# Kernel optimization log

Hardware: AMD Instinct MI355X
Metric: run time of the kernel (lower is better)

Reference implementation:

```python
import jax, jax.numpy as jnp
import numpy as np

NUM_CHANNEL_TYPES = 32  # global channel vocabulary (matches fill_max of channel_idx)


def setup_inputs() -> dict:
    key = jax.random.key(0)
    k1, k2, k3, k4, k5, k6 = jax.random.split(key, 6)
    B, C, H, W, E, P = 32, 8, 224, 224, 768, 16
    return {
        "x": jax.random.normal(k1, (B, C, H, W), dtype=jnp.float32),
        "channel_idx": jax.random.randint(k2, (B, C), 0, NUM_CHANNEL_TYPES, dtype=jnp.int64),
        "proj_w": jax.random.normal(k3, (E, P, P), dtype=jnp.float32) * 0.02,
        "proj_b": jax.random.normal(k4, (E,), dtype=jnp.float32) * 0.02,
        "ctx_w": jax.random.normal(k5, (E, E), dtype=jnp.float32) * 0.02,
        "ctx_b": jax.random.normal(k6, (E,), dtype=jnp.float32) * 0.02,
    }


def reference(x, channel_idx, proj_w, proj_b, ctx_w, ctx_b):
    B, C, H, W = x.shape
    E, P, _ = proj_w.shape
    Hp, Wp = H // P, W // P

    # Conv3d(1, E, kernel=(1,P,P), stride=(1,P,P)) == per-channel 2D patchify matmul
    xp = x.reshape(B, C, Hp, P, Wp, P)
    emb = jnp.einsum('bchpwq,epq->bechw', xp, proj_w) + proj_b[None, :, None, None, None]
    # emb: (B, E, C, Hp, Wp)

    # per-(sample, channel) average patch embedding -> (B, C, E)
    av_patch = emb.mean(axis=(3, 4)).transpose(0, 2, 1)
    flat = av_patch.reshape(B * C, E)
    seg = channel_idx.reshape(-1)

    # segment-mean over the batch by channel index (fused scatter-mean)
    sums = jax.ops.segment_sum(flat, seg, num_segments=NUM_CHANNEL_TYPES)
    cnt = jax.ops.segment_sum(jnp.ones((B * C,), flat.dtype), seg, num_segments=NUM_CHANNEL_TYPES)
    means = sums / jnp.maximum(cnt, 1.0)[:, None]
    chan_embed = means[seg].reshape(B, C, E)  # torch computes this under no_grad

    # context projection and broadcast-add back onto patch embeddings
    ctx = chan_embed @ ctx_w.T + ctx_b            # (B, C, E)
    out = emb + ctx.transpose(0, 2, 1)[:, :, :, None, None]

    # flatten(2).transpose(1, 2): (B, C*Hp*Wp, E)
    return out.reshape(B, E, C * Hp * Wp).transpose(0, 2, 1)
```

## Files before the change

kernel.cpp:

```cpp
#include <hip/hip_runtime.h>
#include <hip/hip_bf16.h>

typedef __attribute__((ext_vector_type(8))) short s16x8;
typedef __attribute__((ext_vector_type(4))) float f32x4;
typedef __attribute__((ext_vector_type(8))) unsigned short u16x8;
typedef __attribute__((ext_vector_type(4))) unsigned short u16x4;

static __device__ __forceinline__ unsigned short f2bf(float f) {
  unsigned int u = __float_as_uint(f);
  unsigned int r = u + 0x7fffu + ((u >> 16) & 1u);
  return (unsigned short)(r >> 16);
}
static __device__ __forceinline__ float bf2f(unsigned short s) {
  return __uint_as_float(((unsigned int)s) << 16);
}

static __device__ __forceinline__ void gload16(const void* g, void* l) {
  __builtin_amdgcn_global_load_lds(
      (const __attribute__((address_space(1))) unsigned int*)g,
      (__attribute__((address_space(3))) unsigned int*)l, 16, 0, 0);
}

__global__ __launch_bounds__(256) void k_mega(const float* __restrict__ x,
                                              unsigned short* __restrict__ xbf,
                                              float* __restrict__ avg3,
                                              const float* __restrict__ pw,
                                              unsigned short* __restrict__ pwbf,
                                              const float* __restrict__ cw,
                                              float* __restrict__ cwT) {
  __shared__ __align__(16) char smem[7168];
  int b = blockIdx.x, t = threadIdx.x;
  if (b < 3584) {
    unsigned short* strip = (unsigned short*)smem;
    int bc = b / 14, hp = b - bc * 14;
    const float* img = x + ((size_t)bc * 224 + hp * 16) * 224;
    for (int idx = t; idx < 896; idx += 256) {
      int row = idx / 56, c4 = idx - row * 56;
      float4 v = reinterpret_cast<const float4*>(img + (size_t)row * 224)[c4];
      int wp = c4 >> 2, q0 = (c4 & 3) << 2;
      u16x4 pk = { f2bf(v.x), f2bf(v.y), f2bf(v.z), f2bf(v.w) };
      *(u16x4*)&strip[wp * 256 + row * 16 + q0] = pk;
    }
    __syncthreads();
    float acc = 0.f;
#pragma unroll
    for (int wp = 0; wp < 14; ++wp) acc += bf2f(strip[wp * 256 + t]);
    avg3[((size_t)bc * 14 + hp) * 256 + t] = acc;
    const u16x8* so = (const u16x8*)strip;
    u16x8* go = (u16x8*)(xbf + ((size_t)bc * 196 + hp * 14) * 256);
    for (int i = t; i < 448; i += 256) go[i] = so[i];
  } else if (b < 3776) {
    int i = (b - 3584) * 256 + t;
    float4 v = reinterpret_cast<const float4*>(pw)[i];
    u16x4 pk = { f2bf(v.x), f2bf(v.y), f2bf(v.z), f2bf(v.w) };
    reinterpret_cast<u16x4*>(pwbf)[i] = pk;
  } else {
    float (*tile)[33] = (float(*)[33])smem;
    int bid2 = b - 3776;
    int bx = bid2 % 24, by = bid2 / 24;
    int tx = t & 31, ty = t >> 5;
#pragma unroll
    for (int k = 0; k < 4; ++k)
      tile[ty + 8 * k][tx] = cw[(size_t)(by * 32 + ty + 8 * k) * 768 + bx * 32 + tx];
    __syncthreads();
#pragma unroll
    for (int k = 0; k < 4; ++k)
      cwT[(size_t)(bx * 32 + ty + 8 * k) * 768 + by * 32 + tx] = tile[tx][ty + 8 * k];
  }
}

__global__ __launch_bounds__(256) void k_segmean(const float* __restrict__ avg3,
                                                 const int* __restrict__ seg,
                                                 float* __restrict__ sp) {
  __shared__ float red[4][64];
  __shared__ int rcnt[4];
  __shared__ int ssg[256];
  int s = blockIdx.x & 31, kc = blockIdx.x >> 5;
  int t = threadIdx.x;
  int kl = t & 63, slice = t >> 6;
  int k = kc * 64 + kl;
  ssg[t] = seg[t];
  __syncthreads();
  float sum = 0.f; int cnt = 0;
  for (int bc = slice * 64; bc < slice * 64 + 64; ++bc) {
    if (ssg[bc] == s) {
      ++cnt;
      const float* row = avg3 + (size_t)bc * 14 * 256 + k;
#pragma unroll
      for (int hp = 0; hp < 14; ++hp) sum += row[hp * 256];
    }
  }
  red[slice][kl] = sum;
  if (kl == 0) rcnt[slice] = cnt;
  __syncthreads();
  if (t < 64) {
    float tot = red[0][t] + red[1][t] + red[2][t] + red[3][t];
    int c = rcnt[0] + rcnt[1] + rcnt[2] + rcnt[3];
    sp[s * 256 + kc * 64 + t] = tot / (196.0f * (float)(c > 0 ? c : 1));
  }
}

__global__ __launch_bounds__(256) void k_means2(const float* __restrict__ sp,
                                                const float* __restrict__ pw,
                                                const float* __restrict__ pb,
                                                float* __restrict__ means) {
  __shared__ float ssp[256];
  __shared__ float red[8][32];
  int s = blockIdx.x & 31, e0 = (blockIdx.x >> 5) << 5;
  int t = threadIdx.x;
  int e = t & 31, ksl = t >> 5;
  ssp[t] = sp[s * 256 + t];
  __syncthreads();
  const float4* w = reinterpret_cast<const float4*>(pw + (size_t)(e0 + e) * 256 + ksl * 32);
  float a = 0.f;
#pragma unroll
  for (int j = 0; j < 8; ++j) {
    float4 v = w[j];
    int kb = ksl * 32 + j * 4;
    a += v.x * ssp[kb] + v.y * ssp[kb + 1] + v.z * ssp[kb + 2] + v.w * ssp[kb + 3];
  }
  red[ksl][e] = a;
  __syncthreads();
  if (t < 32) {
    float tot = 0.f;
#pragma unroll
    for (int j = 0; j < 8; ++j) tot += red[j][t];
    means[s * 768 + e0 + t] = tot + pb[e0 + t];
  }
}

__global__ __launch_bounds__(256) void k_ctx2(const float* __restrict__ means,
                                              const float* __restrict__ cwT,
                                              const float* __restrict__ cb,
                                              const float* __restrict__ pb,
                                              float* __restrict__ addv) {
  __shared__ float mn[768];
  __shared__ float red[8][32];
  int s = blockIdx.x & 31, e0 = (blockIdx.x >> 5) << 5;
  int t = threadIdx.x;
  int e = t & 31, fsl = t >> 5;
  mn[t] = means[s * 768 + t];
  mn[t + 256] = means[s * 768 + 256 + t];
  mn[t + 512] = means[s * 768 + 512 + t];
  __syncthreads();
  const float* col = cwT + (size_t)fsl * 96 * 768 + e0 + e;
  float a = 0.f;
#pragma unroll 8
  for (int j = 0; j < 96; ++j) a += mn[fsl * 96 + j] * col[(size_t)j * 768];
  red[fsl][e] = a;
  __syncthreads();
  if (t < 32) {
    float tot = 0.f;
#pragma unroll
    for (int j = 0; j < 8; ++j) tot += red[j][t];
    addv[s * 768 + e0 + t] = tot + cb[e0 + t] + pb[e0 + t];
  }
}

__global__ __launch_bounds__(256) void k_gemm(
    const unsigned short* __restrict__ xbf, const unsigned short* __restrict__ wbf,
    const float* __restrict__ addv, const int* __restrict__ seg,
    float* __restrict__ out) {
  __shared__ __align__(16) unsigned short Al[128 * 64];
  __shared__ __align__(16) unsigned short Bl[128 * 64];

  int bid = blockIdx.x;
  int xcd = bid & 7, local = bid >> 3;
  int mb = xcd * 49 + local / 6;
  int nb = local - (local / 6) * 6;
  int m0 = mb << 7, n0 = nb << 7;

  int t = threadIdx.x;
  int wave = t >> 6, lane = t & 63;
  int wm = (wave >> 1) << 6, wn = (wave & 1) << 6;
  int lr = lane & 15, hi = lane >> 4;
  int axor = (lr & 7) << 4;

  int swz = (((lane & 7) ^ ((lane >> 3) & 7)) << 4);
  const char* abase = (const char*)xbf + (size_t)(m0 + (lane >> 3)) * 512 + swz + (size_t)wave * 16384;
  const char* bbase = (const char*)wbf + (size_t)(n0 + (lane >> 3)) * 512 + swz + (size_t)wave * 16384;
  char* adst = (char*)Al + wave * 4096;
  char* bdst = (char*)Bl + wave * 4096;
  const char* Alc = (const char*)Al;
  const char* Blc = (const char*)Bl;

  f32x4 acc[4][4] = {};

  for (int kt = 0; kt < 4; ++kt) {
#pragma unroll
    for (int i = 0; i < 4; ++i) {
      gload16(abase + kt * 128 + i * 4096, adst + i * 1024);
      gload16(bbase + kt * 128 + i * 4096, bdst + i * 1024);
    }
    __syncthreads();
#pragma unroll
    for (int kk = 0; kk < 2; ++kk) {
      s16x8 af[4], bv[4];
      int koff = kk * 64 + hi * 16;
#pragma unroll
      for (int i = 0; i < 4; ++i)
        af[i] = *(const s16x8*)(Alc + (wm + i * 16 + lr) * 128 + (koff ^ axor));
#pragma unroll
      for (int j = 0; j < 4; ++j)
        bv[j] = *(const s16x8*)(Blc + (wn + j * 16 + lr) * 128 + (koff ^ axor));
#pragma unroll
      for (int i = 0; i < 4; ++i)
#pragma unroll
        for (int j = 0; j < 4; ++j)
          acc[i][j] = __builtin_amdgcn_mfma_f32_16x16x32_bf16(bv[j], af[i], acc[i][j], 0, 0, 0);
    }
    __syncthreads();
  }

#pragma unroll
  for (int i = 0; i < 4; ++i) {
    int M = m0 + wm + i * 16 + lr;
    int sgi = seg[M / 196];
    const float* av = addv + (size_t)sgi * 768 + n0 + wn + hi * 4;
    float* orow = out + (size_t)M * 768 + n0 + wn + hi * 4;
#pragma unroll
    for (int j = 0; j < 4; ++j) {
      f32x4 a4 = *(const f32x4*)(av + j * 16);
      f32x4 v = acc[i][j];
      v.x += a4.x; v.y += a4.y; v.z += a4.z; v.w += a4.w;
      *(f32x4*)(orow + j * 16) = v;
    }
  }
}

__global__ void k_cvt_fb(const float* __restrict__ in, unsigned short* __restrict__ o) {
  int i = blockIdx.x * 256 + threadIdx.x;
  float4 v = reinterpret_cast<const float4*>(in)[i];
  u16x4 pk = { f2bf(v.x), f2bf(v.y), f2bf(v.z), f2bf(v.w) };
  reinterpret_cast<u16x4*>(o)[i] = pk;
}

__global__ void k_transpose_fb(const float* __restrict__ in, float* __restrict__ out) {
  __shared__ float tile[32][33];
  int bx = blockIdx.x % 24, by = blockIdx.x / 24;
  int tx = threadIdx.x & 31, ty = threadIdx.x >> 5;
#pragma unroll
  for (int k = 0; k < 4; ++k)
    tile[ty + 8 * k][tx] = in[(size_t)(by * 32 + ty + 8 * k) * 768 + bx * 32 + tx];
  __syncthreads();
#pragma unroll
  for (int k = 0; k < 4; ++k)
    out[(size_t)(bx * 32 + ty + 8 * k) * 768 + by * 32 + tx] = tile[tx][ty + 8 * k];
}

__global__ void k_avgpatch_fb(const float* __restrict__ x, float* __restrict__ avg) {
  int bc = blockIdx.x;
  int k = threadIdx.x;
  int p = k >> 4, q = k & 15;
  const float* base = x + (size_t)bc * 224 * 224;
  float s = 0.f;
  for (int hp = 0; hp < 14; ++hp) {
    const float* row = base + (hp * 16 + p) * 224 + q;
#pragma unroll
    for (int wp = 0; wp < 14; ++wp) s += row[wp * 16];
  }
  avg[bc * 256 + k] = s * (1.0f / 196.0f);
}

__global__ __launch_bounds__(768) void k_chain_fb(const float* __restrict__ avg,
                                                  const int* __restrict__ seg,
                                                  const float* __restrict__ pw,
                                                  const float* __restrict__ pb,
                                                  const float* __restrict__ cwT,
                                                  const float* __restrict__ cb,
                                                  float* __restrict__ addv) {
  __shared__ float sp[256];
  __shared__ float mn[768];
  __shared__ int ssg[256];
  int s = blockIdx.x, t = threadIdx.x;
  if (t < 256) ssg[t] = seg[t];
  __syncthreads();
  if (t < 256) {
    float sum = 0.f; int c = 0;
    for (int bc = 0; bc < 256; ++bc)
      if (ssg[bc] == s) { sum += avg[bc * 256 + t]; ++c; }
    sp[t] = sum / (float)(c > 0 ? c : 1);
  }
  __syncthreads();
  {
    const float4* w = reinterpret_cast<const float4*>(pw + (size_t)t * 256);
    float a = 0.f;
#pragma unroll 8
    for (int k = 0; k < 64; ++k) {
      float4 v = w[k];
      a += v.x * sp[k * 4] + v.y * sp[k * 4 + 1] + v.z * sp[k * 4 + 2] + v.w * sp[k * 4 + 3];
    }
    mn[t] = a + pb[t];
  }
  __syncthreads();
  float a2 = 0.f;
#pragma unroll 8
  for (int f = 0; f < 768; ++f) a2 += mn[f] * cwT[(size_t)f * 768 + t];
  addv[s * 768 + t] = a2 + cb[t] + pb[t];
}

__global__ __launch_bounds__(256) void k_gemm_fb(
    const float* __restrict__ x, const unsigned short* __restrict__ wbf,
    const float* __restrict__ addv, const int* __restrict__ seg,
    float* __restrict__ out) {
  __shared__ unsigned short Al[128][40];
  __shared__ unsigned short Bl[128][40];
  int bid = blockIdx.x;
  int xcd = bid & 7, local = bid >> 3;
  int mb = xcd * 49 + local / 6;
  int nb = local - (local / 6) * 6;
  int m0 = mb << 7, n0 = nb << 7;
  int t = threadIdx.x;
  int wave = t >> 6, lane = t & 63;
  int wm = (wave >> 1) << 6, wn = (wave & 1) << 6;
  int lr = lane & 15, lk = (lane >> 4) << 3;
  int mstage = m0 + (t >> 1);
  int halfA = t & 1;
  int bc = mstage / 196;
  int pij = mstage - bc * 196;
  int hp = pij / 14;
  int wp = pij - hp * 14;
  const float* xbase = x + ((size_t)bc * 224 + hp * 16 + halfA) * 224 + wp * 16;
  const unsigned short* bsrc = wbf + (size_t)(n0 + (t >> 1)) * 256 + halfA * 16;
  unsigned short* adst = &Al[t >> 1][halfA * 16];
  unsigned short* bdst = &Bl[t >> 1][halfA * 16];
  f32x4 acc[4][4] = {};
  for (int ks = 0; ks < 8; ++ks) {
    __syncthreads();
    *(u16x8*)bdst       = *(const u16x8*)(bsrc + ks * 32);
    *(u16x8*)(bdst + 8) = *(const u16x8*)(bsrc + ks * 32 + 8);
    {
      const float4* src = reinterpret_cast<const float4*>(xbase + ks * 448);
      float4 v0 = src[0], v1 = src[1], v2 = src[2], v3 = src[3];
      u16x8 p0 = { f2bf(v0.x), f2bf(v0.y), f2bf(v0.z), f2bf(v0.w),
                   f2bf(v1.x), f2bf(v1.y), f2bf(v1.z), f2bf(v1.w) };
      u16x8 p1 = { f2bf(v2.x), f2bf(v2.y), f2bf(v2.z), f2bf(v2.w),
                   f2bf(v3.x), f2bf(v3.y), f2bf(v3.z), f2bf(v3.w) };
      *(u16x8*)adst = p0;
      *(u16x8*)(adst + 8) = p1;
    }
    __syncthreads();
    s16x8 af[4], bfv[4];
#pragma unroll
    for (int i = 0; i < 4; ++i) af[i] = *(const s16x8*)&Al[wm + i * 16 + lr][lk];
#pragma unroll
    for (int j = 0; j < 4; ++j) bfv[j] = *(const s16x8*)&Bl[wn + j * 16 + lr][lk];
#pragma unroll
    for (int i = 0; i < 4; ++i)
#pragma unroll
      for (int j = 0; j < 4; ++j)
        acc[i][j] = __builtin_amdgcn_mfma_f32_16x16x32_bf16(bfv[j], af[i], acc[i][j], 0, 0, 0);
  }
#pragma unroll
  for (int i = 0; i < 4; ++i) {
    int M = m0 + wm + i * 16 + lr;
    int sgi = seg[M / 196];
    int hi = lane >> 4;
    const float* av = addv + (size_t)sgi * 768 + n0 + wn + hi * 4;
    float* orow = out + (size_t)M * 768 + n0 + wn + hi * 4;
#pragma unroll
    for (int j = 0; j < 4; ++j) {
      f32x4 a4 = *(const f32x4*)(av + j * 16);
      f32x4 v = acc[i][j];
      v.x += a4.x; v.y += a4.y; v.z += a4.z; v.w += a4.w;
      *(f32x4*)(orow + j * 16) = v;
    }
  }
}


extern "C" void kernel_launch(void* const* d_in, const int* in_sizes, int n_in,
                              void* d_out, int out_size, void* d_ws, size_t ws_size,
                              hipStream_t stream) {
  (void)in_sizes; (void)n_in; (void)out_size;
  const float* x  = (const float*)d_in[0];
  const int*   sg = (const int*)d_in[1];
  const float* pw = (const float*)d_in[2];
  const float* pb = (const float*)d_in[3];
  const float* cw = (const float*)d_in[4];
  const float* cb = (const float*)d_in[5];
  float* out = (float*)d_out;

  char* ws = (char*)d_ws;
  unsigned short* pwbf = (unsigned short*)ws;
  float* cwT   = (float*)(ws + 393216);
  float* addv  = (float*)(ws + 2752512);
  float* sp    = (float*)(ws + 2850816);
  float* means = (float*)(ws + 2883584);
  float* avg3  = (float*)(ws + 2981888);
  unsigned short* xbf = (unsigned short*)(ws + 6651904);
  const size_t NEED = 6651904u + 25690112u;

  if (ws_size >= NEED) {
    k_mega<<<4352, 256, 0, stream>>>(x, xbf, avg3, pw, pwbf, cw, cwT);
    k_segmean<<<128, 256, 0, stream>>>(avg3, sg, sp);
    k_means2<<<768, 256, 0, stream>>>(sp, pw, pb, means);
    k_ctx2<<<768, 256, 0, stream>>>(means, cwT, cb, pb, addv);
    k_gemm<<<2352, 256, 0, stream>>>(xbf, pwbf, addv, sg, out);
  } else {
    float* avgp = (float*)(ws + 2981888);
    k_cvt_fb<<<192, 256, 0, stream>>>(pw, pwbf);
    k_transpose_fb<<<576, 256, 0, stream>>>(cw, cwT);
    k_avgpatch_fb<<<256, 256, 0, stream>>>(x, avgp);
    k_chain_fb<<<32, 768, 0, stream>>>(avgp, sg, pw, pb, cwT, cb, addv);
    k_gemm_fb<<<2352, 256, 0, stream>>>(x, pwbf, addv, sg, out);
  }
}
```

Before: 87.86 us.

## Double-buffer GEMM K-tiles, pad patch strip in LDS, use nontemporal output stores

The GEMM main loop now uses two 32-wide K buffers in LDS and prefetches the next K slice while computing the current one. This replaces four 64-wide stages that each loaded and then synchronized with nothing overlapping. The LDS swizzle is reworked for the 64-byte row pitch. The patch strip in the conversion kernel gets 272-element padding per patch to reduce LDS bank conflicts, and output stores become nontemporal to avoid polluting the cache. The trade-offs are more barriers (eight iterations instead of four) and smaller MFMA bursts per sync.

New measurement: 101.1 us. 1.15x slower.

```diff
diff --git a/kernel.cpp b/kernel.cpp
--- a/kernel.cpp
+++ b/kernel.cpp
@@ -28,7 +28,7 @@
                                               unsigned short* __restrict__ pwbf,
                                               const float* __restrict__ cw,
                                               float* __restrict__ cwT) {
-  __shared__ __align__(16) char smem[7168];
+  __shared__ __align__(16) char smem[14 * 272 * 2];
   int b = blockIdx.x, t = threadIdx.x;
   if (b < 3584) {
     unsigned short* strip = (unsigned short*)smem;
@@ -39,16 +39,19 @@
       float4 v = reinterpret_cast<const float4*>(img + (size_t)row * 224)[c4];
       int wp = c4 >> 2, q0 = (c4 & 3) << 2;
       u16x4 pk = { f2bf(v.x), f2bf(v.y), f2bf(v.z), f2bf(v.w) };
-      *(u16x4*)&strip[wp * 256 + row * 16 + q0] = pk;
+      *(u16x4*)&strip[wp * 272 + row * 16 + q0] = pk;
     }
     __syncthreads();
     float acc = 0.f;
 #pragma unroll
-    for (int wp = 0; wp < 14; ++wp) acc += bf2f(strip[wp * 256 + t]);
+    for (int wp = 0; wp < 14; ++wp) acc += bf2f(strip[wp * 272 + t]);
     avg3[((size_t)bc * 14 + hp) * 256 + t] = acc;
-    const u16x8* so = (const u16x8*)strip;
-    u16x8* go = (u16x8*)(xbf + ((size_t)bc * 196 + hp * 14) * 256);
-    for (int i = t; i < 448; i += 256) go[i] = so[i];
+    unsigned short* orow = xbf + ((size_t)bc * 196 + hp * 14) * 256;
+    for (int i = t; i < 448; i += 256) {
+      int patch = i >> 5, rem = i & 31;
+      u16x8 v = *(const u16x8*)&strip[patch * 272 + (rem >> 1) * 16 + (rem & 1) * 8];
+      *(u16x8*)(orow + i * 8) = v;
+    }
   } else if (b < 3776) {
     int i = (b - 3584) * 256 + t;
     float4 v = reinterpret_cast<const float4*>(pw)[i];
@@ -161,8 +164,8 @@
     const unsigned short* __restrict__ xbf, const unsigned short* __restrict__ wbf,
     const float* __restrict__ addv, const int* __restrict__ seg,
     float* __restrict__ out) {
-  __shared__ __align__(16) unsigned short Al[128 * 64];
-  __shared__ __align__(16) unsigned short Bl[128 * 64];
+  __shared__ __align__(16) unsigned short Al[2][128 * 32];
+  __shared__ __align__(16) unsigned short Bl[2][128 * 32];
 
   int bid = blockIdx.x;
   int xcd = bid & 7, local = bid >> 3;
@@ -174,41 +177,45 @@
   int wave = t >> 6, lane = t & 63;
   int wm = (wave >> 1) << 6, wn = (wave & 1) << 6;
   int lr = lane & 15, hi = lane >> 4;
-  int axor = (lr & 7) << 4;
-
-  int swz = (((lane & 7) ^ ((lane >> 3) & 7)) << 4);
-  const char* abase = (const char*)xbf + (size_t)(m0 + (lane >> 3)) * 512 + swz + (size_t)wave * 16384;
-  const char* bbase = (const char*)wbf + (size_t)(n0 + (lane >> 3)) * 512 + swz + (size_t)wave * 16384;
-  char* adst = (char*)Al + wave * 4096;
-  char* bdst = (char*)Bl + wave * 4096;
-  const char* Alc = (const char*)Al;
-  const char* Blc = (const char*)Bl;
+
+  int qswz = (lane & 3) ^ ((lane >> 2) & 3);
+  const char* abase = (const char*)xbf + (size_t)(m0 + wave * 32 + (lane >> 2)) * 512 + qswz * 16;
+  const char* bbase = (const char*)wbf + (size_t)(n0 + wave * 32 + (lane >> 2)) * 512 + qswz * 16;
+  int ldso = wave * 2048;
 
   f32x4 acc[4][4] = {};
 
-  for (int kt = 0; kt < 4; ++kt) {
-#pragma unroll
-    for (int i = 0; i < 4; ++i) {
-      gload16(abase + kt * 128 + i * 4096, adst + i * 1024);
-      gload16(bbase + kt * 128 + i * 4096, bdst + i * 1024);
-    }
-    __syncthreads();
-#pragma unroll
-    for (int kk = 0; kk < 2; ++kk) {
-      s16x8 af[4], bv[4];
-      int koff = kk * 64 + hi * 16;
-#pragma unroll
-      for (int i = 0; i < 4; ++i)
-        af[i] = *(const s16x8*)(Alc + (wm + i * 16 + lr) * 128 + (koff ^ axor));
+  gload16(abase, (char*)Al[0] + ldso);
+  gload16(abase + 8192, (char*)Al[0] + ldso + 1024);
+  gload16(bbase, (char*)Bl[0] + ldso);
+  gload16(bbase + 8192, (char*)Bl[0] + ldso + 1024);
+  __syncthreads();
+
+#pragma unroll
+  for (int kt = 0; kt < 8; ++kt) {
+    int cur = kt & 1;
+    if (kt < 7) {
+      int nxt = cur ^ 1;
+      const char* an = abase + (kt + 1) * 64;
+      const char* bn = bbase + (kt + 1) * 64;
+      gload16(an, (char*)Al[nxt] + ldso);
+      gload16(an + 8192, (char*)Al[nxt] + ldso + 1024);
+      gload16(bn, (char*)Bl[nxt] + ldso);
+      gload16(bn + 8192, (char*)Bl[nxt] + ldso + 1024);
+    }
+    s16x8 af[4], bv[4];
+    int qa = (hi ^ (lr & 3)) << 4;
+#pragma unroll
+    for (int i = 0; i < 4; ++i)
+      af[i] = *(const s16x8*)((const char*)Al[cur] + (wm + i * 16 + lr) * 64 + qa);
+#pragma unroll
+    for (int j = 0; j < 4; ++j)
+      bv[j] = *(const s16x8*)((const char*)Bl[cur] + (wn + j * 16 + lr) * 64 + qa);
+#pragma unroll
+    for (int i = 0; i < 4; ++i)
 #pragma unroll
       for (int j = 0; j < 4; ++j)
-        bv[j] = *(const s16x8*)(Blc + (wn + j * 16 + lr) * 128 + (koff ^ axor));
-#pragma unroll
-      for (int i = 0; i < 4; ++i)
-#pragma unroll
-        for (int j = 0; j < 4; ++j)
-          acc[i][j] = __builtin_amdgcn_mfma_f32_16x16x32_bf16(bv[j], af[i], acc[i][j], 0, 0, 0);
-    }
+        acc[i][j] = __builtin_amdgcn_mfma_f32_16x16x32_bf16(bv[j], af[i], acc[i][j], 0, 0, 0);
     __syncthreads();
   }
 
@@ -223,7 +230,7 @@
       f32x4 a4 = *(const f32x4*)(av + j * 16);
       f32x4 v = acc[i][j];
       v.x += a4.x; v.y += a4.y; v.z += a4.z; v.w += a4.w;
-      *(f32x4*)(orow + j * 16) = v;
+      __builtin_nontemporal_store(v, (f32x4*)(orow + j * 16));
     }
   }
 }
```
